# Kernel tuning notes

Measured on AMD Instinct MI355X. Metric: run time of the kernel, lower is better.

The kernel has to match this reference:

```python
import jax, jax.numpy as jnp
import numpy as np

B, H, W, C = 16, 64, 64, 192
NH, WS, SHIFT = 6, 8, 4          # heads, window size, shift (window//2)
DEPTH, MLP_R = 2, 4
N = WS * WS                      # tokens per window = 64
HD = C // NH                     # head dim = 32
SCALE = HD ** -0.5
TBL = (2 * WS - 1) ** 2          # relative-bias table size = 225
NW = (H // WS) * (W // WS)       # windows per image = 64


def _rel_pos_index():
    coords = np.stack(np.meshgrid(np.arange(WS), np.arange(WS), indexing='ij')).reshape(2, -1)
    rel = (coords[:, :, None] - coords[:, None, :]).transpose(1, 2, 0)
    rel[..., 0] += WS - 1
    rel[..., 1] += WS - 1
    rel[..., 0] *= 2 * WS - 1
    return jnp.asarray(rel.sum(-1))  # [N, N] int


def _attn_mask():
    # Swin shifted-window mask: region ids then pairwise -100 where ids differ.
    img = np.zeros((H, W))
    sl = (slice(0, -WS), slice(-WS, -SHIFT), slice(-SHIFT, None))
    cnt = 0
    for hs in sl:
        for ws in sl:
            img[hs, ws] = cnt
            cnt += 1
    mw = img.reshape(H // WS, WS, W // WS, WS).transpose(0, 2, 1, 3).reshape(-1, N)
    diff = mw[:, None, :] - mw[:, :, None]
    return jnp.asarray(np.where(diff != 0, -100.0, 0.0).astype(np.float32))  # [NW, N, N]


REL_IDX = _rel_pos_index()
ATTN_MASK = _attn_mask()


def _ln(x, g, b, eps=1e-5):
    mu = x.mean(-1, keepdims=True)
    var = ((x - mu) ** 2).mean(-1, keepdims=True)
    return (x - mu) * jax.lax.rsqrt(var + eps) * g + b


def setup_inputs() -> dict:
    key = jax.random.key(0)
    ks = jax.random.split(key, 8)
    s = 0.02
    return {
        'x': jax.random.normal(ks[0], (B, H * W, C), jnp.float32),
        'norm1_g': jnp.ones((DEPTH, C)), 'norm1_b': jnp.zeros((DEPTH, C)),
        'qkv_w': jax.random.normal(ks[1], (DEPTH, 3 * C, C)) * s,
        'qkv_b': jnp.zeros((DEPTH, 3 * C)),
        'bias_table': jax.random.normal(ks[2], (DEPTH, TBL, NH)) * s,
        'proj_w': jax.random.normal(ks[3], (DEPTH, C, C)) * s,
        'proj_b': jnp.zeros((DEPTH, C)),
        'norm2_g': jnp.ones((DEPTH, C)), 'norm2_b': jnp.zeros((DEPTH, C)),
        'fc1_w': jax.random.normal(ks[4], (DEPTH, MLP_R * C, C)) * s,
        'fc1_b': jnp.zeros((DEPTH, MLP_R * C)),
        'fc2_w': jax.random.normal(ks[5], (DEPTH, C, MLP_R * C)) * s,
        'fc2_b': jnp.zeros((DEPTH, C)),
    }


def _block(x, shift, n1g, n1b, qw, qb, tbl, pw, pb, n2g, n2b, f1w, f1b, f2w, f2b):
    shortcut = x
    y = _ln(x, n1g, n1b).reshape(B, H, W, C)
    if shift > 0:
        y = jnp.roll(y, (-shift, -shift), axis=(1, 2))
    # window partition -> [B*NW, N, C]
    win = y.reshape(B, H // WS, WS, W // WS, WS, C).transpose(0, 1, 3, 2, 4, 5).reshape(-1, N, C)
    qkv = (win @ qw.T + qb).reshape(-1, N, 3, NH, HD).transpose(2, 0, 3, 1, 4)
    q, k, v = qkv[0] * SCALE, qkv[1], qkv[2]          # each [B*NW, NH, N, HD]
    attn = jnp.einsum('bhnd,bhmd->bhnm', q, k)
    attn = attn + tbl[REL_IDX].transpose(2, 0, 1)[None]  # relative position bias
    if shift > 0:
        attn = (attn.reshape(B, NW, NH, N, N) + ATTN_MASK[None, :, None]).reshape(-1, NH, N, N)
    attn = jax.nn.softmax(attn, axis=-1)
    o = jnp.einsum('bhnm,bhmd->bhnd', attn, v).transpose(0, 2, 1, 3).reshape(-1, N, C)
    o = o @ pw.T + pb
    # window reverse
    y = o.reshape(B, H // WS, W // WS, WS, WS, C).transpose(0, 1, 3, 2, 4, 5).reshape(B, H, W, C)
    if shift > 0:
        y = jnp.roll(y, (shift, shift), axis=(1, 2))
    x = shortcut + y.reshape(B, H * W, C)
    h = _ln(x, n2g, n2b)
    h = jax.nn.gelu(h @ f1w.T + f1b, approximate=False)  # torch nn.GELU = exact erf
    return x + (h @ f2w.T + f2b)


def reference(x, norm1_g, norm1_b, qkv_w, qkv_b, bias_table, proj_w, proj_b,
              norm2_g, norm2_b, fc1_w, fc1_b, fc2_w, fc2_b):
    for i in range(DEPTH):
        shift = 0 if i % 2 == 0 else SHIFT
        x = _block(x, shift, norm1_g[i], norm1_b[i], qkv_w[i], qkv_b[i], bias_table[i],
                   proj_w[i], proj_b[i], norm2_g[i], norm2_b[i],
                   fc1_w[i], fc1_b[i], fc2_w[i], fc2_b[i])
    return x
```

## Files before the change

kernel.cpp:

```cpp
#include <hip/hip_runtime.h>
#include <hip/hip_bf16.h>
#include <math.h>

typedef __hip_bfloat16 bf16;
typedef short bf16x8 __attribute__((ext_vector_type(8)));
typedef short s16x4 __attribute__((ext_vector_type(4)));
typedef float f32x4 __attribute__((ext_vector_type(4)));

#define TOKENS 65536
#define C_ 192

__device__ __forceinline__ float b2f(bf16 v){ return __bfloat162float(v); }
__device__ __forceinline__ bf16 f2b(float v){ return __float2bfloat16(v); }
__device__ __forceinline__ short f2s(float v){
  bf16 b = __float2bfloat16(v);
  union { bf16 b; short s; } u; u.b = b; return u.s;
}
__device__ __forceinline__ float s2f(short s){
  union { unsigned u; float f; } c; c.u = ((unsigned)(unsigned short)s) << 16; return c.f;
}

struct WPtrs { const void* p[13]; };
#define W_TOTAL_ 892480
#define NELEM_ (TOKENS*C_)
__global__ void convert_k(WPtrs wp, const void* __restrict__ x,
                          bf16* __restrict__ canon, float* __restrict__ xf){
  const int offs[13] = {0, 384, 768, 221952, 223104, 225856, 299584,
                        299968, 300352, 300736, 595648, 597184, 892096};
  const int lens[13] = {384, 384, 221184, 1152, 2700, 73728, 384,
                        384, 384, 294912, 1536, 294912, 384};
  int flag = (*(const unsigned*)wp.p[0] == 0x3F800000u) ? 1 : 0;
  int i = blockIdx.x*blockDim.x + threadIdx.x;
  if (i < W_TOTAL_){
    int t = 0;
    while (t < 12 && i >= offs[t+1]) t++;
    int j = i - offs[t];
    if (j < lens[t]){
      if (flag) canon[i] = f2b(((const float*)wp.p[t])[j]);
      else      canon[i] = ((const bf16*)wp.p[t])[j];
    }
  } else {
    int j = i - W_TOTAL_;
    if (j < NELEM_){
      if (flag) xf[j] = ((const float*)x)[j];
      else      xf[j] = b2f(((const bf16*)x)[j]);
    }
  }
}
__global__ void outconv_k(const float* __restrict__ x, void* __restrict__ y, int n,
                          const unsigned* __restrict__ g){
  int flag = (g[0] == 0x3F800000u) ? 1 : 0;
  int i = blockIdx.x*blockDim.x + threadIdx.x;
  if (i >= n) return;
  if (flag) ((float*)y)[i] = x[i];
  else      ((bf16*)y)[i]  = f2b(x[i]);
}

__global__ void setup_k(const bf16* __restrict__ bt, float* __restrict__ biasF,
                        const bf16* __restrict__ f1w, const bf16* __restrict__ f2w,
                        bf16* __restrict__ w1p, bf16* __restrict__ w2p){
  int idx = blockIdx.x*blockDim.x + threadIdx.x;
  if (idx < 2*6*64*64){
    int v = idx & 63;
    int lane = (idx >> 6) & 63;
    int rest = idx >> 12;
    int head = rest % 6, dd = rest / 6;
    int jt = v >> 4, it = (v >> 2) & 3, r = v & 3;
    int quad = lane >> 4, lr = lane & 15;
    int j = jt*16 + quad*4 + r;
    int i = it*16 + lr;
    int rel = ((i>>3) - (j>>3) + 7)*15 + ((i&7) - (j&7) + 7);
    biasF[idx] = b2f(bt[(dd*225 + rel)*6 + head]);
    return;
  }
  int id = idx - 2*6*64*64;
  if (id >= 589824) return;
  int arr = id / 294912;
  int r = id % 294912;
  int d = r / 147456;
  int e = r % 147456;
  int j = e & 7, lane = (e >> 3) & 63, frag = e >> 9;
  int lr = lane & 15, quad = lane >> 4;
  if (arr == 0){
    int ks = frag % 6, t = frag / 6;
    int mh = t & 1, cc = t >> 1;
    w1p[(size_t)d*147456 + e] =
        f1w[(size_t)d*147456 + (size_t)(cc*32 + mh*16 + lr)*192 + ks*32 + quad*8 + j];
  } else {
    int ct = frag % 12, cc = frag / 12;
    w2p[(size_t)d*147456 + e] =
        f2w[(size_t)d*147456 + (size_t)(ct*16 + lr)*768 + cc*32 + quad*8 + j];
  }
}

__global__ __launch_bounds__(768, 1) void attn_fused_k(float* __restrict__ xres,
    const bf16* __restrict__ n1g, const bf16* __restrict__ n1b,
    const bf16* __restrict__ qw, const bf16* __restrict__ qb,
    const bf16* __restrict__ pw, const bf16* __restrict__ pb,
    const float* __restrict__ biasF, int shift)
{
  extern __shared__ char smem[];
  short* xo = (short*)smem;
  int win = blockIdx.x;
  int tid = threadIdx.x;
  int wave = tid >> 6, lane = tid & 63;
  int quad = lane >> 4, lr = lane & 15;
  int head = wave >> 1, half = wave & 1;
  int b_ = win >> 6, wl = win & 63, wh = wl >> 3, wwi = wl & 7;
  short* kh  = (short*)(smem + 25600 + head*18432);
  short* vth = kh + 2560;
  short* qP  = vth + 2304;

  int c0 = lane*3;
  float g0 = b2f(n1g[c0]), g1 = b2f(n1g[c0+1]), g2 = b2f(n1g[c0+2]);
  float e0 = b2f(n1b[c0]), e1 = b2f(n1b[c0+1]), e2 = b2f(n1b[c0+2]);
  #pragma unroll
  for (int p = 0; p < 6; p++){
    int tok = p*12 + wave;
    if (tok < 64){
      int hh = (wh*8 + (tok>>3) + shift) & 63, ww = (wwi*8 + (tok&7) + shift) & 63;
      const float* rowp = xres + ((size_t)(b_<<12) + (hh<<6) + ww)*C_;
      float v0 = rowp[c0], v1 = rowp[c0+1], v2 = rowp[c0+2];
      float s = v0+v1+v2;
      #pragma unroll
      for (int off=32; off; off>>=1) s += __shfl_xor(s, off);
      float mu = s * (1.0f/192.0f);
      float d0=v0-mu, d1=v1-mu, d2=v2-mu;
      float q = d0*d0+d1*d1+d2*d2;
      #pragma unroll
      for (int off=32; off; off>>=1) q += __shfl_xor(q, off);
      float rstd = rsqrtf(q*(1.0f/192.0f) + 1e-5f);
      xo[tok*200 + c0]   = f2s(d0*rstd*g0 + e0);
      xo[tok*200 + c0+1] = f2s(d1*rstd*g1 + e1);
      xo[tok*200 + c0+2] = f2s(d2*rstd*g2 + e2);
    }
  }
  __syncthreads();

  const short* qwd = (const short*)qw;
  #pragma unroll
  for (int cc = 0; cc < 3; cc++){
    int nbase = cc*192 + head*32;
    f32x4 acc[2][2];
    #pragma unroll
    for (int mt = 0; mt < 2; mt++)
      #pragma unroll
      for (int nt = 0; nt < 2; nt++) acc[mt][nt] = (f32x4){0.f,0.f,0.f,0.f};
    #pragma unroll
    for (int ks = 0; ks < 6; ks++){
      bf16x8 af[2], bx[2];
      #pragma unroll
      for (int mt = 0; mt < 2; mt++)
        af[mt] = *(const bf16x8*)(qwd + (size_t)(nbase + mt*16 + lr)*192 + ks*32 + quad*8);
      #pragma unroll
      for (int nt = 0; nt < 2; nt++)
        bx[nt] = *(const bf16x8*)&xo[((2*half + nt)*16 + lr)*200 + ks*32 + quad*8];
      #pragma unroll
      for (int mt = 0; mt < 2; mt++)
        #pragma unroll
        for (int nt = 0; nt < 2; nt++)
          acc[mt][nt] = __builtin_amdgcn_mfma_f32_16x16x32_bf16(af[mt], bx[nt], acc[mt][nt], 0, 0, 0);
    }
    #pragma unroll
    for (int mt = 0; mt < 2; mt++){
      float bv[4];
      #pragma unroll
      for (int r = 0; r < 4; r++) bv[r] = b2f(qb[nbase + mt*16 + quad*4 + r]);
      #pragma unroll
      for (int nt = 0; nt < 2; nt++){
        int tok = (2*half + nt)*16 + lr;
        if (cc == 0){
          s16x4 pk;
          #pragma unroll
          for (int r = 0; r < 4; r++) pk[r] = f2s((acc[mt][nt][r] + bv[r]) * 0.17677669529663689f);
          *(s16x4*)&qP[tok*40 + mt*16 + quad*4] = pk;
        } else if (cc == 1){
          s16x4 pk;
          #pragma unroll
          for (int r = 0; r < 4; r++) pk[r] = f2s(acc[mt][nt][r] + bv[r]);
          *(s16x4*)&kh[tok*40 + mt*16 + quad*4] = pk;
        } else {
          #pragma unroll
          for (int r = 0; r < 4; r++)
            vth[(mt*16 + quad*4 + r)*72 + tok] = f2s(acc[mt][nt][r] + bv[r]);
        }
      }
    }
  }
  __syncthreads();

  bf16x8 ak[4], bq[2];
  #pragma unroll
  for (int jt = 0; jt < 4; jt++) ak[jt] = *(const bf16x8*)&kh[(jt*16 + lr)*40 + quad*8];
  #pragma unroll
  for (int it = 0; it < 2; it++)
    bq[it] = *(const bf16x8*)&qP[((2*half + it)*16 + lr)*40 + quad*8];
  __syncthreads();

  f32x4 S[4][2];
  #pragma unroll
  for (int jt = 0; jt < 4; jt++)
    #pragma unroll
    for (int it = 0; it < 2; it++) S[jt][it] = (f32x4){0.f,0.f,0.f,0.f};
  #pragma unroll
  for (int jt = 0; jt < 4; jt++)
    #pragma unroll
    for (int it = 0; it < 2; it++)
      S[jt][it] = __builtin_amdgcn_mfma_f32_16x16x32_bf16(ak[jt], bq[it], S[jt][it], 0, 0, 0);

  const f32x4* bm = (const f32x4*)(biasF + ((size_t)head*64 + lane)*64);
  #pragma unroll
  for (int jt = 0; jt < 4; jt++)
    #pragma unroll
    for (int it = 0; it < 2; it++) S[jt][it] += bm[jt*4 + 2*half + it];

  if (shift){
    int idi[2];
    #pragma unroll
    for (int it = 0; it < 2; it++){
      int itg = 2*half + it;
      int hh = wh*8 + itg*2 + (lr >> 3);
      int wwc = wwi*8 + (lr & 7);
      idi[it] = (hh < 56 ? 0 : (hh < 60 ? 1 : 2))*3 + (wwc < 56 ? 0 : (wwc < 60 ? 1 : 2));
    }
    #pragma unroll
    for (int jt = 0; jt < 4; jt++)
      #pragma unroll
      for (int r = 0; r < 4; r++){
        int j = jt*16 + quad*4 + r;
        int hh = wh*8 + (j >> 3), wwc = wwi*8 + (j & 7);
        int idj = (hh < 56 ? 0 : (hh < 60 ? 1 : 2))*3 + (wwc < 56 ? 0 : (wwc < 60 ? 1 : 2));
        #pragma unroll
        for (int it = 0; it < 2; it++)
          if (idj != idi[it]) S[jt][it][r] -= 100.f;
      }
  }
  #pragma unroll
  for (int it = 0; it < 2; it++){
    float m = -1e30f;
    #pragma unroll
    for (int jt = 0; jt < 4; jt++)
      #pragma unroll
      for (int r = 0; r < 4; r++) m = fmaxf(m, S[jt][it][r]);
    m = fmaxf(m, __shfl_xor(m, 16));
    m = fmaxf(m, __shfl_xor(m, 32));
    float s = 0.f;
    #pragma unroll
    for (int jt = 0; jt < 4; jt++)
      #pragma unroll
      for (int r = 0; r < 4; r++){
        float e = __expf(S[jt][it][r] - m);
        S[jt][it][r] = e; s += e;
      }
    s += __shfl_xor(s, 16);
    s += __shfl_xor(s, 32);
    float inv = 1.0f / s;
    #pragma unroll
    for (int jt = 0; jt < 4; jt++){
      s16x4 pk;
      #pragma unroll
      for (int r = 0; r < 4; r++) pk[r] = f2s(S[jt][it][r] * inv);
      *(s16x4*)&qP[((2*half + it)*16 + lr)*68 + jt*16 + quad*4] = pk;
    }
  }
  __syncthreads();

  bf16x8 va[2][2], pv[2][2];
  #pragma unroll
  for (int mt = 0; mt < 2; mt++)
    #pragma unroll
    for (int ks = 0; ks < 2; ks++)
      va[mt][ks] = *(const bf16x8*)&vth[(mt*16 + lr)*72 + ks*32 + quad*8];
  #pragma unroll
  for (int nt = 0; nt < 2; nt++)
    #pragma unroll
    for (int ks = 0; ks < 2; ks++)
      pv[nt][ks] = *(const bf16x8*)&qP[((2*half + nt)*16 + lr)*68 + ks*32 + quad*8];

  f32x4 O[2][2];
  #pragma unroll
  for (int mt = 0; mt < 2; mt++)
    #pragma unroll
    for (int nt = 0; nt < 2; nt++) O[mt][nt] = (f32x4){0.f,0.f,0.f,0.f};
  #pragma unroll
  for (int mt = 0; mt < 2; mt++)
    #pragma unroll
    for (int nt = 0; nt < 2; nt++)
      #pragma unroll
      for (int ks = 0; ks < 2; ks++)
        O[mt][nt] = __builtin_amdgcn_mfma_f32_16x16x32_bf16(va[mt][ks], pv[nt][ks], O[mt][nt], 0, 0, 0);

  #pragma unroll
  for (int mt = 0; mt < 2; mt++)
    #pragma unroll
    for (int nt = 0; nt < 2; nt++){
      s16x4 pk;
      #pragma unroll
      for (int r = 0; r < 4; r++) pk[r] = f2s(O[mt][nt][r]);
      *(s16x4*)&xo[((2*half + nt)*16 + lr)*200 + head*32 + mt*16 + quad*4] = pk;
    }
  __syncthreads();

  int wm = wave / 6, wn = wave % 6;
  f32x4 po[2][2];
  #pragma unroll
  for (int mt = 0; mt < 2; mt++)
    #pragma unroll
    for (int nt = 0; nt < 2; nt++) po[mt][nt] = (f32x4){0.f,0.f,0.f,0.f};
  const short* pwd = (const short*)pw;
  #pragma unroll
  for (int ks = 0; ks < 6; ks++){
    bf16x8 ao[2], bw[2];
    #pragma unroll
    for (int mt = 0; mt < 2; mt++)
      ao[mt] = *(const bf16x8*)&xo[(wm*32 + mt*16 + lr)*200 + ks*32 + quad*8];
    #pragma unroll
    for (int nt = 0; nt < 2; nt++)
      bw[nt] = *(const bf16x8*)(pwd + (size_t)(wn*32 + nt*16 + lr)*192 + ks*32 + quad*8);
    #pragma unroll
    for (int mt = 0; mt < 2; mt++)
      #pragma unroll
      for (int nt = 0; nt < 2; nt++)
        po[mt][nt] = __builtin_amdgcn_mfma_f32_16x16x32_bf16(ao[mt], bw[nt], po[mt][nt], 0, 0, 0);
  }
  #pragma unroll
  for (int nt = 0; nt < 2; nt++){
    int n = wn*32 + nt*16 + lr;
    float bv = b2f(pb[n]);
    #pragma unroll
    for (int mt = 0; mt < 2; mt++){
      #pragma unroll
      for (int r = 0; r < 4; r++){
        int tok = wm*32 + mt*16 + quad*4 + r;
        int hh = (wh*8 + (tok>>3) + shift) & 63, ww = (wwi*8 + (tok&7) + shift) & 63;
        float* dst = xres + ((size_t)(b_<<12) + (hh<<6) + ww)*C_ + n;
        *dst += po[mt][nt][r] + bv;
      }
    }
  }
}

__global__ __launch_bounds__(512, 4) void mlp_coop_k(float* __restrict__ xres,
    const bf16* __restrict__ n2g, const bf16* __restrict__ n2b,
    const bf16* __restrict__ w1p, const bf16* __restrict__ f1b,
    const bf16* __restrict__ w2p, const bf16* __restrict__ f2bv)
{
  __shared__ short Wst[2][24*512];
  __shared__ short HsAll[8][16*36];
  int tid = threadIdx.x;
  int wave = tid >> 6, lane = tid & 63;
  int quad = lane >> 4, lr = lane & 15;
  short* Hs = HsAll[wave];
  int t0 = blockIdx.x*128 + wave*16;

  const short* w1 = (const short*)w1p;
  const short* w2 = (const short*)w2p;

  int f0 = wave*3;

  bf16x8 rg[3];
  #pragma unroll
  for (int k = 0; k < 3; k++){
    int f = f0 + k;
    const short* g = (f < 12) ? (w1 + (size_t)f*512 + lane*8)
                              : (w2 + (size_t)(f - 12)*512 + lane*8);
    rg[k] = *(const bf16x8*)g;
  }

  bf16x8 xh[6];
  {
    const float* rowp = xres + (size_t)(t0 + lr)*C_;
    float v[6][8];
    float s = 0.f;
    #pragma unroll
    for (int ks = 0; ks < 6; ks++){
      int cb = ks*32 + quad*8;
      #pragma unroll
      for (int j = 0; j < 8; j++){ v[ks][j] = rowp[cb+j]; s += v[ks][j]; }
    }
    s += __shfl_xor(s, 16); s += __shfl_xor(s, 32);
    float mu = s*(1.0f/192.0f);
    float q = 0.f;
    #pragma unroll
    for (int ks = 0; ks < 6; ks++)
      #pragma unroll
      for (int j = 0; j < 8; j++){ float d = v[ks][j]-mu; q += d*d; }
    q += __shfl_xor(q, 16); q += __shfl_xor(q, 32);
    float rstd = rsqrtf(q*(1.0f/192.0f) + 1e-5f);
    #pragma unroll
    for (int ks = 0; ks < 6; ks++){
      int cb = ks*32 + quad*8;
      #pragma unroll
      for (int j = 0; j < 8; j++)
        xh[ks][j] = f2s((v[ks][j]-mu)*rstd*b2f(n2g[cb+j]) + b2f(n2b[cb+j]));
    }
  }

  #pragma unroll
  for (int k = 0; k < 3; k++)
    *(bf16x8*)&Wst[0][(f0 + k)*512 + lane*8] = rg[k];

  f32x4 acc[12];
  #pragma unroll
  for (int ct = 0; ct < 12; ct++) acc[ct] = (f32x4){0.f,0.f,0.f,0.f};

  int cur = 0;
  for (int cc = 0; cc < 24; cc++){
    if (cc < 23){
      #pragma unroll
      for (int k = 0; k < 3; k++){
        int f = f0 + k;
        const short* g = (f < 12) ? (w1 + (size_t)((cc+1)*12 + f)*512 + lane*8)
                                  : (w2 + (size_t)((cc+1)*12 + (f - 12))*512 + lane*8);
        rg[k] = *(const bf16x8*)g;
      }
    }

    __syncthreads();

    const short* rdb = &Wst[cur][0];

    f32x4 hacc[2];
    hacc[0] = (f32x4){0.f,0.f,0.f,0.f};
    hacc[1] = (f32x4){0.f,0.f,0.f,0.f};
    #pragma unroll
    for (int ks = 0; ks < 6; ks++){
      bf16x8 af0 = *(const bf16x8*)&rdb[ks*512 + lane*8];
      bf16x8 af1 = *(const bf16x8*)&rdb[(6 + ks)*512 + lane*8];
      hacc[0] = __builtin_amdgcn_mfma_f32_16x16x32_bf16(af0, xh[ks], hacc[0], 0, 0, 0);
      hacc[1] = __builtin_amdgcn_mfma_f32_16x16x32_bf16(af1, xh[ks], hacc[1], 0, 0, 0);
    }
    #pragma unroll
    for (int mh = 0; mh < 2; mh++){
      s16x4 bb = *(const s16x4*)((const short*)f1b + cc*32 + mh*16 + quad*4);
      s16x4 pk;
      #pragma unroll
      for (int r = 0; r < 4; r++){
        float x = hacc[mh][r] + s2f(bb[r]);
        float y = x*(0.7978845608f + 0.0356774081f*x*x);
        float t = __expf(2.0f*fminf(y, 9.0f));
        pk[r] = f2s(x*t/(t + 1.0f));
      }
      *(s16x4*)&Hs[lr*36 + mh*16 + quad*4] = pk;
    }
    bf16x8 ah = *(const bf16x8*)&Hs[lr*36 + quad*8];
    #pragma unroll
    for (int ct = 0; ct < 12; ct++){
      bf16x8 bw = *(const bf16x8*)&rdb[(12 + ct)*512 + lane*8];
      acc[ct] = __builtin_amdgcn_mfma_f32_16x16x32_bf16(bw, ah, acc[ct], 0, 0, 0);
    }

    if (cc < 23){
      #pragma unroll
      for (int k = 0; k < 3; k++)
        *(bf16x8*)&Wst[cur ^ 1][(f0 + k)*512 + lane*8] = rg[k];
    }
    cur ^= 1;
  }

  {
    int m = t0 + lr;
    float* rowd = xres + (size_t)m*C_;
    #pragma unroll
    for (int ct = 0; ct < 12; ct++){
      int n0 = ct*16 + quad*4;
      s16x4 bb = *(const s16x4*)((const short*)f2bv + n0);
      f32x4* dst = (f32x4*)(rowd + n0);
      f32x4 cur4 = *dst;
      #pragma unroll
      for (int r = 0; r < 4; r++) cur4[r] += acc[ct][r] + s2f(bb[r]);
      *dst = cur4;
    }
  }
}

extern "C" void kernel_launch(void* const* d_in, const int* in_sizes, int n_in,
                              void* d_out, int out_size, void* d_ws, size_t ws_size,
                              hipStream_t stream)
{
  (void)in_sizes; (void)n_in; (void)out_size;

  if (ws_size < (size_t)52117000) return;
  char* ws = (char*)d_ws;
  float* xf   = (float*)ws;
  bf16* canon = (bf16*)(ws + 50331648);
  float* biasF = (float*)d_out;
  bf16* w1p = (bf16*)((char*)d_out + 196608);
  bf16* w2p = (bf16*)((char*)d_out + 786432);

  static const int W_OFF[13] = {0, 384, 768, 221952, 223104, 225856, 299584,
                                299968, 300352, 300736, 595648, 597184, 892096};

  hipFuncSetAttribute((const void*)attn_fused_k,
                      hipFuncAttributeMaxDynamicSharedMemorySize, 136192);

  WPtrs wp;
  for (int i = 0; i < 13; i++) wp.p[i] = d_in[i+1];

  const int nelem = TOKENS*C_;
  convert_k<<<(W_TOTAL_ + nelem + 255)/256, 256, 0, stream>>>(wp, d_in[0], canon, xf);

  const bf16* n1g = canon + W_OFF[0];
  const bf16* n1b = canon + W_OFF[1];
  const bf16* qw  = canon + W_OFF[2];
  const bf16* qb  = canon + W_OFF[3];
  const bf16* bt  = canon + W_OFF[4];
  const bf16* pw  = canon + W_OFF[5];
  const bf16* pb  = canon + W_OFF[6];
  const bf16* n2g = canon + W_OFF[7];
  const bf16* n2b = canon + W_OFF[8];
  const bf16* f1w = canon + W_OFF[9];
  const bf16* f1b = canon + W_OFF[10];
  const bf16* f2w = canon + W_OFF[11];
  const bf16* f2bv= canon + W_OFF[12];

  setup_k<<<(49152 + 589824 + 255)/256, 256, 0, stream>>>(bt, biasF, f1w, f2w, w1p, w2p);

  for (int d = 0; d < 2; d++){
    int shift = d ? 4 : 0;
    attn_fused_k<<<1024, 768, 136192, stream>>>(xf,
        n1g + d*192, n1b + d*192, qw + d*576*192, qb + d*576,
        pw + d*192*192, pb + d*192, biasF + d*6*64*64, shift);
    mlp_coop_k<<<512, 512, 0, stream>>>(xf,
        n2g + d*192, n2b + d*192, w1p + d*147456, f1b + d*768,
        w2p + d*147456, f2bv + d*192);
  }
  outconv_k<<<nelem/256, 256, 0, stream>>>(xf, d_out, nelem, (const unsigned*)d_in[1]);
}
```

Baseline: 575.7 us.

## Give each MLP wave 32 tokens so every staged weight fragment feeds two MFMAs

The MLP kernel now runs 4 waves per block instead of 8, and each wave handles 32 tokens as two 16-token tiles. Each wave stages 6 weight fragments per chunk into shared memory. Every weight fragment read from LDS now drives two MFMAs, halving LDS weight reads per FLOP and amortising the per-chunk barrier over more work. In exchange, register pressure roughly doubles (accumulators, LN'd inputs, prefetched weights) and there are fewer waves per block, which may cut occupancy and latency hiding.

Result: faster. 561.9 us (-2.4%).

```diff
diff --git a/kernel.cpp b/kernel.cpp
--- a/kernel.cpp
+++ b/kernel.cpp
@@ -340,36 +340,37 @@
   }
 }
 
-__global__ __launch_bounds__(512, 4) void mlp_coop_k(float* __restrict__ xres,
+__global__ __launch_bounds__(256, 2) void mlp_coop32_k(float* __restrict__ xres,
     const bf16* __restrict__ n2g, const bf16* __restrict__ n2b,
     const bf16* __restrict__ w1p, const bf16* __restrict__ f1b,
     const bf16* __restrict__ w2p, const bf16* __restrict__ f2bv)
 {
   __shared__ short Wst[2][24*512];
-  __shared__ short HsAll[8][16*36];
+  __shared__ short HsAll[4][32*36];
   int tid = threadIdx.x;
   int wave = tid >> 6, lane = tid & 63;
   int quad = lane >> 4, lr = lane & 15;
   short* Hs = HsAll[wave];
-  int t0 = blockIdx.x*128 + wave*16;
+  int t0 = blockIdx.x*128 + wave*32;
 
   const short* w1 = (const short*)w1p;
   const short* w2 = (const short*)w2p;
 
-  int f0 = wave*3;
-
-  bf16x8 rg[3];
-  #pragma unroll
-  for (int k = 0; k < 3; k++){
+  int f0 = wave*6;
+
+  bf16x8 rg[6];
+  #pragma unroll
+  for (int k = 0; k < 6; k++){
     int f = f0 + k;
     const short* g = (f < 12) ? (w1 + (size_t)f*512 + lane*8)
                               : (w2 + (size_t)(f - 12)*512 + lane*8);
     rg[k] = *(const bf16x8*)g;
   }
 
-  bf16x8 xh[6];
-  {
-    const float* rowp = xres + (size_t)(t0 + lr)*C_;
+  bf16x8 xh[2][6];
+  #pragma unroll
+  for (int nt = 0; nt < 2; nt++){
+    const float* rowp = xres + (size_t)(t0 + nt*16 + lr)*C_;
     float v[6][8];
     float s = 0.f;
     #pragma unroll
@@ -392,23 +393,25 @@
       int cb = ks*32 + quad*8;
       #pragma unroll
       for (int j = 0; j < 8; j++)
-        xh[ks][j] = f2s((v[ks][j]-mu)*rstd*b2f(n2g[cb+j]) + b2f(n2b[cb+j]));
-    }
-  }
-
-  #pragma unroll
-  for (int k = 0; k < 3; k++)
+        xh[nt][ks][j] = f2s((v[ks][j]-mu)*rstd*b2f(n2g[cb+j]) + b2f(n2b[cb+j]));
+    }
+  }
+
+  #pragma unroll
+  for (int k = 0; k < 6; k++)
     *(bf16x8*)&Wst[0][(f0 + k)*512 + lane*8] = rg[k];
 
-  f32x4 acc[12];
-  #pragma unroll
-  for (int ct = 0; ct < 12; ct++) acc[ct] = (f32x4){0.f,0.f,0.f,0.f};
+  f32x4 acc[12][2];
+  #pragma unroll
+  for (int ct = 0; ct < 12; ct++)
+    #pragma unroll
+    for (int nt = 0; nt < 2; nt++) acc[ct][nt] = (f32x4){0.f,0.f,0.f,0.f};
 
   int cur = 0;
   for (int cc = 0; cc < 24; cc++){
     if (cc < 23){
       #pragma unroll
-      for (int k = 0; k < 3; k++){
+      for (int k = 0; k < 6; k++){
         int f = f0 + k;
         const short* g = (f < 12) ? (w1 + (size_t)((cc+1)*12 + f)*512 + lane*8)
                                   : (w2 + (size_t)((cc+1)*12 + (f - 12))*512 + lane*8);
@@ -420,46 +423,56 @@
 
     const short* rdb = &Wst[cur][0];
 
-    f32x4 hacc[2];
-    hacc[0] = (f32x4){0.f,0.f,0.f,0.f};
-    hacc[1] = (f32x4){0.f,0.f,0.f,0.f};
+    f32x4 hacc[2][2];
+    #pragma unroll
+    for (int mh = 0; mh < 2; mh++)
+      #pragma unroll
+      for (int nt = 0; nt < 2; nt++) hacc[mh][nt] = (f32x4){0.f,0.f,0.f,0.f};
     #pragma unroll
     for (int ks = 0; ks < 6; ks++){
       bf16x8 af0 = *(const bf16x8*)&rdb[ks*512 + lane*8];
       bf16x8 af1 = *(const bf16x8*)&rdb[(6 + ks)*512 + lane*8];
-      hacc[0] = __builtin_amdgcn_mfma_f32_16x16x32_bf16(af0, xh[ks], hacc[0], 0, 0, 0);
-      hacc[1] = __builtin_amdgcn_mfma_f32_16x16x32_bf16(af1, xh[ks], hacc[1], 0, 0, 0);
+      hacc[0][0] = __builtin_amdgcn_mfma_f32_16x16x32_bf16(af0, xh[0][ks], hacc[0][0], 0, 0, 0);
+      hacc[0][1] = __builtin_amdgcn_mfma_f32_16x16x32_bf16(af0, xh[1][ks], hacc[0][1], 0, 0, 0);
+      hacc[1][0] = __builtin_amdgcn_mfma_f32_16x16x32_bf16(af1, xh[0][ks], hacc[1][0], 0, 0, 0);
+      hacc[1][1] = __builtin_amdgcn_mfma_f32_16x16x32_bf16(af1, xh[1][ks], hacc[1][1], 0, 0, 0);
     }
     #pragma unroll
     for (int mh = 0; mh < 2; mh++){
       s16x4 bb = *(const s16x4*)((const short*)f1b + cc*32 + mh*16 + quad*4);
-      s16x4 pk;
-      #pragma unroll
-      for (int r = 0; r < 4; r++){
-        float x = hacc[mh][r] + s2f(bb[r]);
-        float y = x*(0.7978845608f + 0.0356774081f*x*x);
-        float t = __expf(2.0f*fminf(y, 9.0f));
-        pk[r] = f2s(x*t/(t + 1.0f));
+      #pragma unroll
+      for (int nt = 0; nt < 2; nt++){
+        s16x4 pk;
+        #pragma unroll
+        for (int r = 0; r < 4; r++){
+          float x = hacc[mh][nt][r] + s2f(bb[r]);
+          float y = x*(0.7978845608f + 0.0356774081f*x*x);
+          float t = __expf(2.0f*fminf(y, 9.0f));
+          pk[r] = f2s(x*t/(t + 1.0f));
+        }
+        *(s16x4*)&Hs[(nt*16 + lr)*36 + mh*16 + quad*4] = pk;
       }
-      *(s16x4*)&Hs[lr*36 + mh*16 + quad*4] = pk;
-    }
-    bf16x8 ah = *(const bf16x8*)&Hs[lr*36 + quad*8];
+    }
+    bf16x8 ah0 = *(const bf16x8*)&Hs[lr*36 + quad*8];
+    bf16x8 ah1 = *(const bf16x8*)&Hs[(16 + lr)*36 + quad*8];
     #pragma unroll
     for (int ct = 0; ct < 12; ct++){
       bf16x8 bw = *(const bf16x8*)&rdb[(12 + ct)*512 + lane*8];
-      acc[ct] = __builtin_amdgcn_mfma_f32_16x16x32_bf16(bw, ah, acc[ct], 0, 0, 0);
+      acc[ct][0] = __builtin_amdgcn_mfma_f32_16x16x32_bf16(bw, ah0, acc[ct][0], 0, 0, 0);
+      acc[ct][1] = __builtin_amdgcn_mfma_f32_16x16x32_bf16(bw, ah1, acc[ct][1], 0, 0, 0);
     }
 
     if (cc < 23){
       #pragma unroll
-      for (int k = 0; k < 3; k++)
+      for (int k = 0; k < 6; k++)
         *(bf16x8*)&Wst[cur ^ 1][(f0 + k)*512 + lane*8] = rg[k];
     }
     cur ^= 1;
   }
 
-  {
-    int m = t0 + lr;
+  #pragma unroll
+  for (int nt = 0; nt < 2; nt++){
+    int m = t0 + nt*16 + lr;
     float* rowd = xres + (size_t)m*C_;
     #pragma unroll
     for (int ct = 0; ct < 12; ct++){
@@ -468,7 +481,7 @@
       f32x4* dst = (f32x4*)(rowd + n0);
       f32x4 cur4 = *dst;
       #pragma unroll
-      for (int r = 0; r < 4; r++) cur4[r] += acc[ct][r] + s2f(bb[r]);
+      for (int r = 0; r < 4; r++) cur4[r] += acc[ct][nt][r] + s2f(bb[r]);
       *dst = cur4;
     }
   }
@@ -521,7 +534,7 @@
     attn_fused_k<<<1024, 768, 136192, stream>>>(xf,
         n1g + d*192, n1b + d*192, qw + d*576*192, qb + d*576,
         pw + d*192*192, pb + d*192, biasF + d*6*64*64, shift);
-    mlp_coop_k<<<512, 512, 0, stream>>>(xf,
+    mlp_coop32_k<<<512, 256, 0, stream>>>(xf,
         n2g + d*192, n2b + d*192, w1p + d*147456, f1b + d*768,
         w2p + d*147456, f2bv + d*192);
   }
```
